# Performance work log

Measured on AMD Instinct MI355X. Metric: run time of the kernel, lower is better.

Reference implementation:

```python
import jax, jax.numpy as jnp
import numpy as np
from jax import lax

B, N, W, L, H = 8, 1024, 1024, 12, 16
EPS = 1e-5


def setup_inputs() -> dict:
    key = jax.random.key(0)
    ks = jax.random.split(key, 14)
    std = 0.25 / np.sqrt(W)  # init_scale * sqrt(1/width)
    inp = {
        "x": jax.random.normal(ks[0], (B, N, W), dtype=jnp.float32),
        # stacked per-layer params, leading dim L
        "ln1_g": jnp.ones((L, W), jnp.float32),
        "ln1_b": jnp.zeros((L, W), jnp.float32),
        "w_qkv": jax.random.normal(ks[1], (L, W, 3 * W), jnp.float32) * std,
        "b_qkv": jnp.zeros((L, 3 * W), jnp.float32),
        "w_o":   jax.random.normal(ks[2], (L, W, W), jnp.float32) * std,
        "b_o":   jnp.zeros((L, W), jnp.float32),
        "ln2_g": jnp.ones((L, W), jnp.float32),
        "ln2_b": jnp.zeros((L, W), jnp.float32),
        "w_fc":  jax.random.normal(ks[3], (L, W, 4 * W), jnp.float32) * std,
        "b_fc":  jnp.zeros((L, 4 * W), jnp.float32),
        "w_pr":  jax.random.normal(ks[4], (L, 4 * W, W), jnp.float32) * std,
        "b_pr":  jnp.zeros((L, W), jnp.float32),
    }
    return inp


def _layernorm(x, g, b):
    mu = jnp.mean(x, axis=-1, keepdims=True)
    var = jnp.mean(jnp.square(x - mu), axis=-1, keepdims=True)
    return (x - mu) * lax.rsqrt(var + EPS) * g + b


def _attention(qkv, heads):
    # qkv: [B, N, 3W]; matches QKVMultiheadAttention exactly
    bs, n_ctx, width3 = qkv.shape
    attn_ch = width3 // heads // 3
    scale = 1.0 / np.sqrt(np.sqrt(attn_ch))
    qkv = qkv.reshape(bs, n_ctx, heads, 3 * attn_ch)
    q, k, v = jnp.split(qkv, 3, axis=-1)  # each [B,N,H,c]
    w = jnp.einsum("bthc,bshc->bhts", q * scale, k * scale)
    w = jax.nn.softmax(w.astype(jnp.float32), axis=-1).astype(qkv.dtype)
    out = jnp.einsum("bhts,bshc->bthc", w, v)
    return out.reshape(bs, n_ctx, heads * attn_ch)


def reference(x, ln1_g, ln1_b, w_qkv, b_qkv, w_o, b_o,
              ln2_g, ln2_b, w_fc, b_fc, w_pr, b_pr):
    params = (ln1_g, ln1_b, w_qkv, b_qkv, w_o, b_o,
              ln2_g, ln2_b, w_fc, b_fc, w_pr, b_pr)

    def step(h, p):
        (g1, bb1, wqkv, bqkv, wo, bo, g2, bb2, wfc, bfc, wpr, bpr) = p
        a = _layernorm(h, g1, bb1)
        a = jnp.einsum("bnw,wk->bnk", a, wqkv) + bqkv
        a = _attention(a, H)
        a = jnp.einsum("bnw,wk->bnk", a, wo) + bo
        h = h + a
        m = _layernorm(h, g2, bb2)
        m = jax.nn.gelu(jnp.einsum("bnw,wf->bnf", m, wfc) + bfc, approximate=False)
        m = jnp.einsum("bnf,fw->bnw", m, wpr) + bpr
        return h + m, None

    out, _ = lax.scan(step, x, params)
    return out
```

## Files before the change

kernel.cpp:

```cpp
#include <hip/hip_runtime.h>
#include <cstdint>
#include <cstddef>

#define WDIM 1024
#define BDIM 8
#define NDIM 1024
#define LDIM 12
#define HDIM 16
#define MROWS (BDIM * NDIM)

using bf16x8 = __attribute__((ext_vector_type(8))) __bf16;
using f32x4  = __attribute__((ext_vector_type(4))) float;
using u16x8  = __attribute__((ext_vector_type(8))) ushort;

static __device__ __forceinline__ f32x4 mfma16(bf16x8 a, bf16x8 b, f32x4 c) {
  return __builtin_amdgcn_mfma_f32_16x16x32_bf16(a, b, c, 0, 0, 0);
}

static __device__ __forceinline__ ushort f2bf(float f) {
  uint32_t u = __builtin_bit_cast(uint32_t, f);
  u = (u + 0x7FFFu + ((u >> 16) & 1u)) >> 16;
  return (ushort)u;
}

static __device__ __forceinline__ void g2lds16(const void* g, void* l) {
  __builtin_amdgcn_global_load_lds(
      (__attribute__((address_space(1))) void*)(g),
      (__attribute__((address_space(3))) void*)(l), 16, 0, 0);
}

__global__ __launch_bounds__(256) void ln_kernel(const float* __restrict__ h,
                                                 const float* __restrict__ g,
                                                 const float* __restrict__ b,
                                                 ushort* __restrict__ out) {
  const int row = blockIdx.x;
  const int tid = threadIdx.x;
  const float4 v = ((const float4*)(h + (size_t)row * WDIM))[tid];
  float s  = v.x + v.y + v.z + v.w;
  float s2 = v.x * v.x + v.y * v.y + v.z * v.z + v.w * v.w;
  for (int off = 32; off; off >>= 1) {
    s  += __shfl_xor(s, off);
    s2 += __shfl_xor(s2, off);
  }
  __shared__ float red[8];
  const int w = tid >> 6;
  if ((tid & 63) == 0) { red[w] = s; red[4 + w] = s2; }
  __syncthreads();
  s  = red[0] + red[1] + red[2] + red[3];
  s2 = red[4] + red[5] + red[6] + red[7];
  const float mu   = s * (1.0f / WDIM);
  const float var  = s2 * (1.0f / WDIM) - mu * mu;
  const float rstd = rsqrtf(var + 1e-5f);
  const float4 gv = ((const float4*)g)[tid];
  const float4 bv = ((const float4*)b)[tid];
  ushort4 o;
  o.x = f2bf((v.x - mu) * rstd * gv.x + bv.x);
  o.y = f2bf((v.y - mu) * rstd * gv.y + bv.y);
  o.z = f2bf((v.z - mu) * rstd * gv.z + bv.z);
  o.w = f2bf((v.w - mu) * rstd * gv.w + bv.w);
  ((ushort4*)(out + (size_t)row * WDIM))[tid] = o;
}

__global__ __launch_bounds__(256) void transpose_cvt(const float* __restrict__ in,
                                                     ushort* __restrict__ out,
                                                     int K, int N) {
  __shared__ float sm[32][33];
  const int n0 = blockIdx.x * 32, k0 = blockIdx.y * 32;
  const int tx = threadIdx.x, ty = threadIdx.y;
  #pragma unroll
  for (int j = 0; j < 4; ++j)
    sm[ty + j * 8][tx] = in[(size_t)(k0 + ty + j * 8) * N + n0 + tx];
  __syncthreads();
  #pragma unroll
  for (int j = 0; j < 4; ++j)
    out[(size_t)(n0 + ty + j * 8) * K + k0 + tx] = f2bf(sm[tx][ty + j * 8]);
}

__global__ __launch_bounds__(256) void v_transpose(const ushort* __restrict__ qkv,
                                                   ushort* __restrict__ vT) {
  const int nb = blockIdx.x, bh = blockIdx.y;
  const int b = bh >> 4, h = bh & 15;
  const int tid = threadIdx.x;
  __shared__ ushort smT[64 * 64];
  const int n0 = nb * 64;
  const size_t rowb = (size_t)b * NDIM;
  #pragma unroll
  for (int p = 0; p < 2; ++p) {
    const int n  = p * 32 + (tid >> 3);
    const int d0 = (tid & 7) * 8;
    const uint4 vv = *(const uint4*)(qkv + (rowb + n0 + n) * 3072 + h * 192 + 128 + d0);
    const ushort* e = (const ushort*)&vv;
    const int key = d0;
    #pragma unroll
    for (int j = 0; j < 8; ++j)
      smT[(d0 + j) * 64 + (n ^ key)] = e[j];
  }
  __syncthreads();
  #pragma unroll
  for (int p = 0; p < 2; ++p) {
    const int d  = p * 32 + (tid >> 3);
    const int nc = (tid & 7) * 8;
    const int key = (d >> 3) << 3;
    const uint4 ov = *(const uint4*)&smT[d * 64 + (nc ^ key)];
    *(uint4*)(vT + ((size_t)bh * 64 + d) * NDIM + n0 + nc) = ov;
  }
}

enum { EPI_BF16 = 0, EPI_RES = 1, EPI_GELU = 2 };

template <int EPI>
__global__ __launch_bounds__(256) void gemm_kernel(
    const ushort* __restrict__ A, const ushort* __restrict__ Bt,
    const float* __restrict__ bias, float* __restrict__ resid,
    ushort* __restrict__ outb, int M, int N, int K) {
  __shared__ ushort smA[2][128 * 64];
  __shared__ ushort smB[2][128 * 64];
  const int tid = threadIdx.x;
  const int w = tid >> 6, l = tid & 63;
  const int lr = l & 15, lg = l >> 4;
  const int wr = (w >> 1) * 64, wc = (w & 1) * 64;

  const int gx = gridDim.x;
  const int nwg = gx * gridDim.y;
  const int id0 = blockIdx.y * gx + blockIdx.x;
  const int id = (id0 & 7) * (nwg >> 3) + (id0 >> 3);
  const int row0 = (id / gx) * 128, col0 = (id % gx) * 128;

  const int srow = tid >> 3;
  const int sslot = tid & 7;
  f32x4 acc[4][4] = {};
  const int KT = K >> 6;

  auto stage = [&](int buf, int kt) {
    const int kb = kt << 6;
    #pragma unroll
    for (int j = 0; j < 4; ++j) {
      const int r = j * 32 + srow;
      const int sc = ((sslot ^ (r & 7)) * 8);
      g2lds16(A  + (size_t)(row0 + r) * K + kb + sc, &smA[buf][j * 2048 + w * 512]);
      g2lds16(Bt + (size_t)(col0 + r) * K + kb + sc, &smB[buf][j * 2048 + w * 512]);
    }
  };

  stage(0, 0);
  int cur = 0;
  for (int kt = 0; kt < KT; ++kt) {
    __syncthreads();
    if (kt + 1 < KT) stage(cur ^ 1, kt + 1);
    bf16x8 af[2][4], bfr[2][4];
    const int rs = lr & 7;
    #pragma unroll
    for (int kk = 0; kk < 2; ++kk) {
      #pragma unroll
      for (int t = 0; t < 4; ++t) {
        const int k8 = (kk * 4 + lg) ^ rs;
        af[kk][t]  = *(const bf16x8*)&smA[cur][(wr + t * 16 + lr) * 64 + k8 * 8];
        bfr[kk][t] = *(const bf16x8*)&smB[cur][(wc + t * 16 + lr) * 64 + k8 * 8];
      }
    }
    __builtin_amdgcn_s_setprio(1);
    #pragma unroll
    for (int kk = 0; kk < 2; ++kk)
      #pragma unroll
      for (int mt = 0; mt < 4; ++mt)
        #pragma unroll
        for (int nt = 0; nt < 4; ++nt)
          acc[mt][nt] = mfma16(af[kk][mt], bfr[kk][nt], acc[mt][nt]);
    __builtin_amdgcn_s_setprio(0);
    cur ^= 1;
  }

  #pragma unroll
  for (int mt = 0; mt < 4; ++mt) {
    #pragma unroll
    for (int nt = 0; nt < 4; ++nt) {
      #pragma unroll
      for (int i = 0; i < 4; ++i) {
        const int r = row0 + wr + mt * 16 + lg * 4 + i;
        const int c = col0 + wc + nt * 16 + lr;
        float v = acc[mt][nt][i] + bias[c];
        if constexpr (EPI == EPI_RES) {
          resid[(size_t)r * N + c] += v;
        } else if constexpr (EPI == EPI_GELU) {
          const float gg = 0.5f * v * (1.0f + erff(v * 0.70710678118f));
          outb[(size_t)r * N + c] = f2bf(gg);
        } else {
          outb[(size_t)r * N + c] = f2bf(v);
        }
      }
    }
  }
}

__global__ __launch_bounds__(512) void attn_kernel(const ushort* __restrict__ qkv,
                                                   const ushort* __restrict__ vT,
                                                   ushort* __restrict__ out) {
  const int qb = blockIdx.x;
  const int bh = blockIdx.y;
  const int b = bh >> 4, h = bh & 15;
  const int tid = threadIdx.x;
  const int w = tid >> 6, l = tid & 63;
  const int lr = l & 15, lg = l >> 4;
  __shared__ ushort smK[2][64 * 64];
  __shared__ ushort smV[2][64 * 64];
  __shared__ ushort smP[8][16 * 64];
  const int q0 = qb * 128 + w * 16;
  const size_t rowb = (size_t)b * NDIM;
  const ushort* vhead = vT + (size_t)bh * 64 * NDIM;
  ushort* P = smP[w];

  const u16x8 ob = {0x3F80, 0x3F80, 0x3F80, 0x3F80, 0x3F80, 0x3F80, 0x3F80, 0x3F80};
  const bf16x8 onesv = __builtin_bit_cast(bf16x8, ob);

  const int srow = l >> 3;
  const int scol = ((l & 7) ^ srow) * 8;
  const ushort* kg = qkv + (rowb + w * 8 + srow) * 3072 + h * 192 + 64 + scol;
  const ushort* vg = vhead + (size_t)(w * 8 + srow) * NDIM + scol;

  auto stage = [&](int buf, int kb) {
    g2lds16(kg + (size_t)kb * 64 * 3072, &smK[buf][w * 512]);
    g2lds16(vg + kb * 64,                &smV[buf][w * 512]);
  };

  bf16x8 qf0, qf1;
  {
    const ushort* qp = qkv + (rowb + q0 + lr) * 3072 + h * 192;
    qf0 = *(const bf16x8*)(qp + lg * 8);
    qf1 = *(const bf16x8*)(qp + 32 + lg * 8);
  }
  f32x4 o[4] = {};
  f32x4 lacc = {0.f, 0.f, 0.f, 0.f};

  stage(0, 0);
  int cur = 0;
  for (int kb = 0; kb < NDIM / 64; ++kb) {
    __syncthreads();
    if (kb + 1 < NDIM / 64) stage(cur ^ 1, kb + 1);

    const int rs = lr & 7;
    f32x4 s[4];
    #pragma unroll
    for (int kt = 0; kt < 4; ++kt) {
      const ushort* krow = &smK[cur][(kt * 16 + lr) * 64];
      const bf16x8 kf0 = *(const bf16x8*)&krow[(lg ^ rs) * 8];
      const bf16x8 kf1 = *(const bf16x8*)&krow[((4 + lg) ^ rs) * 8];
      f32x4 z = {0.f, 0.f, 0.f, 0.f};
      s[kt] = mfma16(qf1, kf1, mfma16(qf0, kf0, z));
    }

    #pragma unroll
    for (int i = 0; i < 4; ++i) {
      const int row = lg * 4 + i;
      const int swz = (row & 7) << 3;
      ushort* pr = P + row * 64;
      pr[lr ^ swz]        = f2bf(__expf(s[0][i] * 0.125f));
      pr[(16 + lr) ^ swz] = f2bf(__expf(s[1][i] * 0.125f));
      pr[(32 + lr) ^ swz] = f2bf(__expf(s[2][i] * 0.125f));
      pr[(48 + lr) ^ swz] = f2bf(__expf(s[3][i] * 0.125f));
    }

    const int rswz = rs << 3;
    const bf16x8 pf0 = *(const bf16x8*)&P[lr * 64 + ((lg * 8) ^ rswz)];
    const bf16x8 pf1 = *(const bf16x8*)&P[lr * 64 + ((32 + lg * 8) ^ rswz)];
    lacc = mfma16(pf0, onesv, mfma16(pf1, onesv, lacc));
    #pragma unroll
    for (int dt = 0; dt < 4; ++dt) {
      const ushort* vrow = &smV[cur][(dt * 16 + lr) * 64];
      const bf16x8 vf0 = *(const bf16x8*)&vrow[(lg ^ rs) * 8];
      const bf16x8 vf1 = *(const bf16x8*)&vrow[((4 + lg) ^ rs) * 8];
      o[dt] = mfma16(pf0, vf0, mfma16(pf1, vf1, o[dt]));
    }
    cur ^= 1;
  }

  #pragma unroll
  for (int i = 0; i < 4; ++i) {
    const float inv = 1.0f / lacc[i];
    const size_t orow = (rowb + q0 + lg * 4 + i) * (size_t)WDIM;
    #pragma unroll
    for (int dt = 0; dt < 4; ++dt)
      out[orow + h * 64 + dt * 16 + lr] = f2bf(o[dt][i] * inv);
  }
}

extern "C" void kernel_launch(void* const* d_in, const int* in_sizes, int n_in,
                              void* d_out, int out_size, void* d_ws, size_t ws_size,
                              hipStream_t stream) {
  const float* x     = (const float*)d_in[0];
  const float* ln1_g = (const float*)d_in[1];
  const float* ln1_b = (const float*)d_in[2];
  const float* w_qkv = (const float*)d_in[3];
  const float* b_qkv = (const float*)d_in[4];
  const float* w_o   = (const float*)d_in[5];
  const float* b_o   = (const float*)d_in[6];
  const float* ln2_g = (const float*)d_in[7];
  const float* ln2_b = (const float*)d_in[8];
  const float* w_fc  = (const float*)d_in[9];
  const float* b_fc  = (const float*)d_in[10];
  const float* w_pr  = (const float*)d_in[11];
  const float* b_pr  = (const float*)d_in[12];

  float* hbuf = (float*)d_out;

  uint8_t* p = (uint8_t*)d_ws;
  ushort* wqkv_t = (ushort*)p; p += (size_t)3072 * 1024 * 2;
  ushort* wo_t   = (ushort*)p; p += (size_t)1024 * 1024 * 2;
  ushort* wfc_t  = (ushort*)p; p += (size_t)4096 * 1024 * 2;
  ushort* wpr_t  = (ushort*)p; p += (size_t)1024 * 4096 * 2;
  ushort* lnb    = (ushort*)p; p += (size_t)MROWS * 1024 * 2;
  ushort* qkvb   = (ushort*)p; p += (size_t)MROWS * 3072 * 2;
  ushort* attnb  = (ushort*)p; p += (size_t)MROWS * 1024 * 2;
  ushort* mlpb   = (ushort*)p; p += (size_t)MROWS * 4096 * 2;
  ushort* vTb    = (ushort*)p; p += (size_t)BDIM * HDIM * 64 * NDIM * 2;

  hipMemcpyAsync(hbuf, x, (size_t)MROWS * WDIM * sizeof(float),
                 hipMemcpyDeviceToDevice, stream);

  for (int l = 0; l < LDIM; ++l) {
    ln_kernel<<<MROWS, 256, 0, stream>>>(hbuf, ln1_g + l * 1024, ln1_b + l * 1024, lnb);
    transpose_cvt<<<dim3(3072 / 32, 1024 / 32), dim3(32, 8), 0, stream>>>(
        w_qkv + (size_t)l * 1024 * 3072, wqkv_t, 1024, 3072);
    gemm_kernel<EPI_BF16><<<dim3(24, 64), 256, 0, stream>>>(
        lnb, wqkv_t, b_qkv + (size_t)l * 3072, nullptr, qkvb, MROWS, 3072, 1024);
    v_transpose<<<dim3(16, 128), 256, 0, stream>>>(qkvb, vTb);
    attn_kernel<<<dim3(8, 128), 512, 0, stream>>>(qkvb, vTb, attnb);
    transpose_cvt<<<dim3(32, 32), dim3(32, 8), 0, stream>>>(
        w_o + (size_t)l * 1024 * 1024, wo_t, 1024, 1024);
    gemm_kernel<EPI_RES><<<dim3(8, 64), 256, 0, stream>>>(
        attnb, wo_t, b_o + (size_t)l * 1024, hbuf, nullptr, MROWS, 1024, 1024);
    ln_kernel<<<MROWS, 256, 0, stream>>>(hbuf, ln2_g + l * 1024, ln2_b + l * 1024, lnb);
    transpose_cvt<<<dim3(4096 / 32, 1024 / 32), dim3(32, 8), 0, stream>>>(
        w_fc + (size_t)l * 1024 * 4096, wfc_t, 1024, 4096);
    gemm_kernel<EPI_GELU><<<dim3(32, 64), 256, 0, stream>>>(
        lnb, wfc_t, b_fc + (size_t)l * 4096, nullptr, mlpb, MROWS, 4096, 1024);
    transpose_cvt<<<dim3(1024 / 32, 4096 / 32), dim3(32, 8), 0, stream>>>(
        w_pr + (size_t)l * 4096 * 1024, wpr_t, 4096, 1024);
    gemm_kernel<EPI_RES><<<dim3(8, 64), 256, 0, stream>>>(
        mlpb, wpr_t, b_pr + (size_t)l * 1024, hbuf, nullptr, MROWS, 1024, 4096);
  }
}
```

Before: 4.547 ms.

## Add 256x256-tile 8-wave GEMM with ping-pong LDS pipeline for QKV and FC

Adds a new GEMM kernel with 256x256 output tiles, 512 threads, and a double-buffered LDS schedule. It splits each 64-wide K step into 32-wide halves that are staged asynchronously, interleaved with MFMA phases, and uses s_setprio around the MFMAs. The QKV and FC projections switch to it, which raises arithmetic intensity per workgroup and overlaps global loads with compute. In exchange it needs much higher register pressure (128 accumulators per lane), and the larger tiles give fewer workgroups (384 and 512), which risks lower CU occupancy.

```diff
diff --git a/kernel.cpp b/kernel.cpp
--- a/kernel.cpp
+++ b/kernel.cpp
@@ -109,6 +109,152 @@
 enum { EPI_BF16 = 0, EPI_RES = 1, EPI_GELU = 2 };
 
 template <int EPI>
+__global__ __launch_bounds__(512, 2) void gemm256_kernel(
+    const ushort* __restrict__ A, const ushort* __restrict__ Bt,
+    const float* __restrict__ bias, ushort* __restrict__ outb,
+    int M, int N, int K) {
+  __shared__ ushort smA[2 * 2 * 256 * 32];
+  __shared__ ushort smB[2 * 2 * 256 * 32];
+  const int tid = threadIdx.x;
+  const int w = tid >> 6, l = tid & 63;
+  const int lr = l & 15, lg = l >> 4;
+  const int wm = w >> 2, wn = w & 3;
+
+  const int gx = gridDim.x;
+  const int nwg = gx * gridDim.y;
+  const int id0 = blockIdx.y * gx + blockIdx.x;
+  const int id = (id0 & 7) * (nwg >> 3) + (id0 >> 3);
+  const int row0 = (id / gx) * 256, col0 = (id % gx) * 256;
+
+  const int KT = K >> 6;
+  const int srow_l = l >> 2;
+  const int scol = (((l & 3) ^ ((l >> 3) & 3)) * 8);
+  const int ks = ((lg ^ ((lr >> 1) & 3)) * 8);
+
+  f32x4 acc[8][4] = {};
+
+  auto stageA = [&](int tau, int hh) {
+    const int base = (((tau & 1) * 2 + hh) * 8192);
+    const int colb = tau * 64 + hh * 32 + scol;
+    #pragma unroll
+    for (int j = 0; j < 2; ++j) {
+      const int c = j * 8 + w;
+      g2lds16(A + (size_t)(row0 + 16 * c + srow_l) * K + colb, &smA[base + c * 512]);
+    }
+  };
+  auto stageB = [&](int tau, int hh) {
+    const int base = (((tau & 1) * 2 + hh) * 8192);
+    const int colb = tau * 64 + hh * 32 + scol;
+    #pragma unroll
+    for (int j = 0; j < 2; ++j) {
+      const int c = j * 8 + w;
+      g2lds16(Bt + (size_t)(col0 + 16 * c + srow_l) * K + colb, &smB[base + c * 512]);
+    }
+  };
+
+  stageA(0, 0); stageB(0, 0);
+  stageA(0, 1); stageB(0, 1);
+  stageA(1, 0); stageB(1, 0);
+  asm volatile("s_waitcnt vmcnt(8)" ::: "memory");
+  __builtin_amdgcn_sched_barrier(0);
+  __builtin_amdgcn_s_barrier();
+
+  for (int tau = 0; tau < KT; ++tau) {
+    const int ab0 = (tau & 1) * 16384;
+    const int ab1 = ab0 + 8192;
+    bf16x8 af[8], bf0, bf1;
+
+    #pragma unroll
+    for (int m = 0; m < 8; ++m)
+      af[m] = *(const bf16x8*)&smA[ab0 + (wm * 128 + m * 16 + lr) * 32 + ks];
+    bf0 = *(const bf16x8*)&smB[ab0 + (wn * 64 + lr) * 32 + ks];
+    bf1 = *(const bf16x8*)&smB[ab0 + (wn * 64 + 16 + lr) * 32 + ks];
+    if (tau + 1 < KT) stageA(tau + 1, 1);
+    __builtin_amdgcn_s_barrier();
+    asm volatile("s_waitcnt lgkmcnt(0)" ::: "memory");
+    __builtin_amdgcn_sched_barrier(0);
+    __builtin_amdgcn_s_setprio(1);
+    #pragma unroll
+    for (int m = 0; m < 8; ++m) {
+      acc[m][0] = mfma16(af[m], bf0, acc[m][0]);
+      acc[m][1] = mfma16(af[m], bf1, acc[m][1]);
+    }
+    __builtin_amdgcn_s_setprio(0);
+    __builtin_amdgcn_s_barrier();
+
+    bf0 = *(const bf16x8*)&smB[ab0 + (wn * 64 + 32 + lr) * 32 + ks];
+    bf1 = *(const bf16x8*)&smB[ab0 + (wn * 64 + 48 + lr) * 32 + ks];
+    if (tau + 1 < KT) stageB(tau + 1, 1);
+    __builtin_amdgcn_s_barrier();
+    asm volatile("s_waitcnt lgkmcnt(0)" ::: "memory");
+    __builtin_amdgcn_sched_barrier(0);
+    __builtin_amdgcn_s_setprio(1);
+    #pragma unroll
+    for (int m = 0; m < 8; ++m) {
+      acc[m][2] = mfma16(af[m], bf0, acc[m][2]);
+      acc[m][3] = mfma16(af[m], bf1, acc[m][3]);
+    }
+    __builtin_amdgcn_s_setprio(0);
+    if (tau + 1 < KT) { asm volatile("s_waitcnt vmcnt(8)" ::: "memory"); }
+    else              { asm volatile("s_waitcnt vmcnt(0)" ::: "memory"); }
+    __builtin_amdgcn_sched_barrier(0);
+    __builtin_amdgcn_s_barrier();
+
+    #pragma unroll
+    for (int m = 0; m < 8; ++m)
+      af[m] = *(const bf16x8*)&smA[ab1 + (wm * 128 + m * 16 + lr) * 32 + ks];
+    bf0 = *(const bf16x8*)&smB[ab1 + (wn * 64 + lr) * 32 + ks];
+    bf1 = *(const bf16x8*)&smB[ab1 + (wn * 64 + 16 + lr) * 32 + ks];
+    if (tau + 2 < KT) { stageA(tau + 2, 0); stageB(tau + 2, 0); }
+    __builtin_amdgcn_s_barrier();
+    asm volatile("s_waitcnt lgkmcnt(0)" ::: "memory");
+    __builtin_amdgcn_sched_barrier(0);
+    __builtin_amdgcn_s_setprio(1);
+    #pragma unroll
+    for (int m = 0; m < 8; ++m) {
+      acc[m][0] = mfma16(af[m], bf0, acc[m][0]);
+      acc[m][1] = mfma16(af[m], bf1, acc[m][1]);
+    }
+    __builtin_amdgcn_s_setprio(0);
+    __builtin_amdgcn_s_barrier();
+
+    bf0 = *(const bf16x8*)&smB[ab1 + (wn * 64 + 32 + lr) * 32 + ks];
+    bf1 = *(const bf16x8*)&smB[ab1 + (wn * 64 + 48 + lr) * 32 + ks];
+    __builtin_amdgcn_s_barrier();
+    asm volatile("s_waitcnt lgkmcnt(0)" ::: "memory");
+    __builtin_amdgcn_sched_barrier(0);
+    __builtin_amdgcn_s_setprio(1);
+    #pragma unroll
+    for (int m = 0; m < 8; ++m) {
+      acc[m][2] = mfma16(af[m], bf0, acc[m][2]);
+      acc[m][3] = mfma16(af[m], bf1, acc[m][3]);
+    }
+    __builtin_amdgcn_s_setprio(0);
+    if (tau + 2 < KT)      { asm volatile("s_waitcnt vmcnt(8)" ::: "memory"); }
+    else if (tau + 1 < KT) { asm volatile("s_waitcnt vmcnt(4)" ::: "memory"); }
+    __builtin_amdgcn_sched_barrier(0);
+    __builtin_amdgcn_s_barrier();
+  }
+
+  #pragma unroll
+  for (int m = 0; m < 8; ++m) {
+    #pragma unroll
+    for (int n = 0; n < 4; ++n) {
+      #pragma unroll
+      for (int i = 0; i < 4; ++i) {
+        const int r = row0 + wm * 128 + m * 16 + lg * 4 + i;
+        const int c = col0 + wn * 64 + n * 16 + lr;
+        float v = acc[m][n][i] + bias[c];
+        if constexpr (EPI == EPI_GELU) {
+          v = 0.5f * v * (1.0f + erff(v * 0.70710678118f));
+        }
+        outb[(size_t)r * N + c] = f2bf(v);
+      }
+    }
+  }
+}
+
+template <int EPI>
 __global__ __launch_bounds__(256) void gemm_kernel(
     const ushort* __restrict__ A, const ushort* __restrict__ Bt,
     const float* __restrict__ bias, float* __restrict__ resid,
@@ -320,8 +466,8 @@
     ln_kernel<<<MROWS, 256, 0, stream>>>(hbuf, ln1_g + l * 1024, ln1_b + l * 1024, lnb);
     transpose_cvt<<<dim3(3072 / 32, 1024 / 32), dim3(32, 8), 0, stream>>>(
         w_qkv + (size_t)l * 1024 * 3072, wqkv_t, 1024, 3072);
-    gemm_kernel<EPI_BF16><<<dim3(24, 64), 256, 0, stream>>>(
-        lnb, wqkv_t, b_qkv + (size_t)l * 3072, nullptr, qkvb, MROWS, 3072, 1024);
+    gemm256_kernel<EPI_BF16><<<dim3(12, 32), 512, 0, stream>>>(
+        lnb, wqkv_t, b_qkv + (size_t)l * 3072, qkvb, MROWS, 3072, 1024);
     v_transpose<<<dim3(16, 128), 256, 0, stream>>>(qkvb, vTb);
     attn_kernel<<<dim3(8, 128), 512, 0, stream>>>(qkvb, vTb, attnb);
     transpose_cvt<<<dim3(32, 32), dim3(32, 8), 0, stream>>>(
@@ -331,8 +477,8 @@
     ln_kernel<<<MROWS, 256, 0, stream>>>(hbuf, ln2_g + l * 1024, ln2_b + l * 1024, lnb);
     transpose_cvt<<<dim3(4096 / 32, 1024 / 32), dim3(32, 8), 0, stream>>>(
         w_fc + (size_t)l * 1024 * 4096, wfc_t, 1024, 4096);
-    gemm_kernel<EPI_GELU><<<dim3(32, 64), 256, 0, stream>>>(
-        lnb, wfc_t, b_fc + (size_t)l * 4096, nullptr, mlpb, MROWS, 4096, 1024);
+    gemm256_kernel<EPI_GELU><<<dim3(16, 32), 512, 0, stream>>>(
+        lnb, wfc_t, b_fc + (size_t)l * 4096, mlpb, MROWS, 4096, 1024);
     transpose_cvt<<<dim3(1024 / 32, 4096 / 32), dim3(32, 8), 0, stream>>>(
         w_pr + (size_t)l * 4096 * 1024, wpr_t, 4096, 1024);
     gemm_kernel<EPI_RES><<<dim3(8, 64), 256, 0, stream>>>(
```

Measured after the change: 4.549 ms. About the same (+0.0%).
